# Kernel tuning notes

Hardware: AMD Instinct MI355X
Metric: run time of the kernel (lower is better)

## Reference

```python
import jax, jax.numpy as jnp
import numpy as np

N_E = 16384
E_DIM = 256
BETA = 0.25


def setup_inputs() -> dict:
    key = jax.random.key(0)
    k1, k2 = jax.random.split(key)
    z = jax.random.normal(k1, (8, E_DIM, 32, 32), dtype=jnp.float32)
    embedding = jax.random.uniform(
        k2, (N_E, E_DIM), dtype=jnp.float32, minval=-1.0 / N_E, maxval=1.0 / N_E
    )
    return {"z": z, "embedding": embedding}


def reference(z, embedding):
    # b c h w -> b h w c
    zc = jnp.transpose(z, (0, 2, 3, 1))
    b, h, w, c = zc.shape
    z_flat = zc.reshape(-1, c)  # [N, e_dim]

    # squared-distance matrix: ||z||^2 + ||e||^2 - 2 z e^T  -> [N, n_e]
    d = (
        jnp.sum(z_flat * z_flat, axis=1, keepdims=True)
        + jnp.sum(embedding * embedding, axis=1)
        - 2.0 * jnp.einsum("nd,kd->nk", z_flat, embedding)
    )
    idx = jnp.argmin(d, axis=1)  # [N]

    z_q = embedding[idx].reshape(b, h, w, c)

    sg = jax.lax.stop_gradient
    # legacy=True loss: mse(sg(z_q), z) + beta * mse(z_q, sg(z))
    loss = jnp.mean((sg(z_q) - zc) ** 2) + BETA * jnp.mean((z_q - sg(zc)) ** 2)

    # straight-through estimator
    z_q_st = zc + sg(z_q - zc)
    z_q_out = jnp.transpose(z_q_st, (0, 3, 1, 2))  # b h w c -> b c h w
    return z_q_out, loss, idx
```

## Files before the change

### kernel.cpp

```cpp
#include <hip/hip_runtime.h>

#define E_DIM  256
#define N_E    16384
#define N_ROWS 8192
#define HW     1024
#define NPART  128

typedef _Float16 f16x8 __attribute__((ext_vector_type(8)));
typedef float    f32x4 __attribute__((ext_vector_type(4)));

#define ESCALE   1048576.0f
#define UNSCALE  1.9073486328125e-6f

#define ROR_DPP(v, CTRL) \
  ((unsigned)__builtin_amdgcn_update_dpp(0, (int)(v), (CTRL), 0xF, 0xF, false))

__device__ __forceinline__ float score_ref32(const float* zr,
                                             const float* __restrict__ E,
                                             const float* __restrict__ eNorm,
                                             int idx, float zn) {
  const float4* e4p = (const float4*)(E + (size_t)idx * E_DIM);
  float d0 = 0.f, d1 = 0.f, d2 = 0.f, d3 = 0.f;
#pragma unroll 16
  for (int q = 0; q < 64; ++q) {
    float4 e4 = e4p[q];
    d0 = fmaf(zr[q * 4 + 0], e4.x, d0);
    d1 = fmaf(zr[q * 4 + 1], e4.y, d1);
    d2 = fmaf(zr[q * 4 + 2], e4.z, d2);
    d3 = fmaf(zr[q * 4 + 3], e4.w, d3);
  }
  float dot = (d0 + d1) + (d2 + d3);
  float base = zn + eNorm[idx];
  float td = 2.0f * dot;
  return base - td;
}

#define ZB_Z    256
#define EB_E    512
__global__ __launch_bounds__(256) void k_prep(const float* __restrict__ z,
                                              const float* __restrict__ E,
                                              _Float16* __restrict__ Ah,
                                              _Float16* __restrict__ Bh,
                                              float* __restrict__ eNorm,
                                              float* __restrict__ zNorm,
                                              float* __restrict__ zL1,
                                              float* __restrict__ out_loss) {
#pragma clang fp contract(off)
  const int bi = blockIdx.x, t = threadIdx.x;

  if (bi < ZB_Z) {
    __shared__ float sLZ[256][32];
    __shared__ float sN2[16][32];
    __shared__ float sL1[16][32];
    const int n0 = bi * 32;
    const int b = n0 >> 10, hw0 = n0 & 1023;

    {
      const int nl = t & 31, cs = t >> 5;
      const float* zb = z + (size_t)b * E_DIM * HW + hw0 + nl;
#pragma unroll 4
      for (int it = 0; it < 32; ++it) {
        int c = it * 8 + cs;
        sLZ[c][nl] = zb[(size_t)c * HW];
      }
    }
    __syncthreads();

    {
      const int nl = t & 31, seg = t >> 5;
      const int n = n0 + nl;
      const int perm = (n >> 1) & 3;
#pragma unroll
      for (int u = 0; u < 4; ++u) {
        const int c0 = seg * 32 + u * 8;
        f16x8 hh;
#pragma unroll
        for (int j = 0; j < 8; ++j) hh[j] = (_Float16)sLZ[c0 + j][nl];
        size_t dst = (size_t)seg * (N_ROWS * 32) + (size_t)n * 32 + (size_t)(u ^ perm) * 8;
        *(f16x8*)&Ah[dst] = hh;
      }
    }

#pragma unroll
    for (int it = 0; it < 2; ++it) {
      int task = it * 256 + t;
      int nl = task & 31, c16 = task >> 5;
      int h = c16 >> 3, j = c16 & 7;
      float r2 = 0.f, r1 = 0.f;
#pragma unroll
      for (int i = 0; i < 16; ++i) {
        float v = sLZ[h * 128 + i * 8 + j][nl];
        r2 = r2 + v * v;
        r1 = r1 + fabsf(v);
      }
      sN2[c16][nl] = r2;
      sL1[c16][nl] = r1;
    }
    __syncthreads();
    if (t < 32) {
      float q[16], p[16];
#pragma unroll
      for (int c16 = 0; c16 < 16; ++c16) { q[c16] = sN2[c16][t]; p[c16] = sL1[c16][t]; }
      float h0 = ((q[0] + q[1]) + (q[2] + q[3])) + ((q[4] + q[5]) + (q[6] + q[7]));
      float h1 = ((q[8] + q[9]) + (q[10] + q[11])) + ((q[12] + q[13]) + (q[14] + q[15]));
      zNorm[n0 + t] = h0 + h1;
      float g0 = ((p[0] + p[1]) + (p[2] + p[3])) + ((p[4] + p[5]) + (p[6] + p[7]));
      float g1 = ((p[8] + p[9]) + (p[10] + p[11])) + ((p[12] + p[13]) + (p[14] + p[15]));
      zL1[n0 + t] = g0 + g1;
    }
  } else {
    __shared__ float sNP[8][32];
    const int be = bi - ZB_Z;
    if (be == 0 && t == 0) out_loss[0] = 0.f;
    const int kc = t >> 5, rl = t & 31;
    const int k = be * 32 + rl;
    const int perm = (k >> 1) & 3;
    const float* src = E + (size_t)k * E_DIM + kc * 32;

    float4 v4[8];
#pragma unroll
    for (int u2 = 0; u2 < 8; ++u2) v4[u2] = ((const float4*)src)[u2];

    float nsum = 0.f;
    size_t base = (size_t)kc * (N_E * 32) + (size_t)k * 32;
#pragma unroll
    for (int u = 0; u < 4; ++u) {
      float v[8] = {v4[u * 2].x, v4[u * 2].y, v4[u * 2].z, v4[u * 2].w,
                    v4[u * 2 + 1].x, v4[u * 2 + 1].y, v4[u * 2 + 1].z, v4[u * 2 + 1].w};
      f16x8 hh;
#pragma unroll
      for (int j = 0; j < 8; ++j) {
        nsum = nsum + v[j] * v[j];
        hh[j] = (_Float16)(v[j] * ESCALE);
      }
      *(f16x8*)&Bh[base + (size_t)(u ^ perm) * 8] = hh;
    }
    sNP[kc][rl] = nsum;
    __syncthreads();
    if (t < 32) {
      float s = 0.f;
#pragma unroll
      for (int kc2 = 0; kc2 < 8; ++kc2) s += sNP[kc2][t];
      eNorm[be * 32 + t] = s;
    }
  }
}

__global__ __launch_bounds__(128, 2) void k_scores_mfma(
    const _Float16* __restrict__ Ah, const _Float16* __restrict__ Bh,
    const float* __restrict__ eNorm,
    unsigned* __restrict__ pK1, unsigned* __restrict__ pK2,
    unsigned* __restrict__ pK3) {
#pragma clang fp contract(off)
  const int mt = blockIdx.x, nt = blockIdx.y;
  const int m0 = mt * 128, n0 = nt * 128;

  const int t = threadIdx.x;
  const int lane = t & 63, w = t >> 6;
  const int tx = lane & 15, quad = lane >> 4;
  const int wm = w * 64;
  const int swz = (quad ^ ((tx >> 1) & 3)) * 8;

  const size_t planeA = (size_t)N_ROWS * 32, planeB = (size_t)N_E * 32;
  const size_t baseA = (size_t)(m0 + wm + tx) * 32 + swz;
  const size_t baseB = (size_t)(n0 + tx) * 32 + swz;

  f32x4 acc[4][8];
#pragma unroll
  for (int i = 0; i < 4; ++i)
#pragma unroll
    for (int j = 0; j < 8; ++j) acc[i][j] = (f32x4){0.f, 0.f, 0.f, 0.f};

#pragma unroll
  for (int kc = 0; kc < 8; ++kc) {
    f16x8 ah[4], bh[8];
#pragma unroll
    for (int i = 0; i < 4; ++i)
      ah[i] = *(const f16x8*)&Ah[kc * planeA + baseA + (size_t)i * 512];
#pragma unroll
    for (int j = 0; j < 8; ++j)
      bh[j] = *(const f16x8*)&Bh[kc * planeB + baseB + (size_t)j * 512];

    __builtin_amdgcn_s_setprio(1);
#pragma unroll
    for (int j = 0; j < 8; ++j)
#pragma unroll
      for (int i = 0; i < 4; ++i)
        acc[i][j] = __builtin_amdgcn_mfma_f32_16x16x32_f16(ah[i], bh[j], acc[i][j], 0, 0, 0);
    __builtin_amdgcn_s_setprio(0);
  }

  float enq[8];
#pragma unroll
  for (int j = 0; j < 8; ++j)
    enq[j] = fmaf(eNorm[n0 + j * 16 + tx], 2097152.f, 131072.f);

#pragma unroll
  for (int i = 0; i < 4; ++i) {
#pragma unroll
    for (int r = 0; r < 4; ++r) {
      const int rloc = wm + i * 16 + quad * 4 + r;
      unsigned k[8];
#pragma unroll
      for (int j = 0; j < 8; ++j) {
        float tq = fmaf(acc[i][j][r], -4.0f, enq[j]);
        k[j] = (((unsigned)tq) << 14) | (unsigned)(n0 + j * 16 + tx);
      }
      unsigned a = min(k[0], k[1]), b = max(k[0], k[1]);
      unsigned c = min(k[2], k[3]), d = max(k[2], k[3]);
      unsigned a1 = min(a, c), e0 = max(a, c), f0 = min(b, d);
      unsigned a2 = min(e0, f0), a3 = max(e0, f0);
      a = min(k[4], k[5]); b = max(k[4], k[5]);
      c = min(k[6], k[7]); d = max(k[6], k[7]);
      unsigned b1 = min(a, c); e0 = max(a, c); f0 = min(b, d);
      unsigned b2 = min(e0, f0), b3 = max(e0, f0);
      unsigned m1 = min(a1, b1);
      unsigned m2 = min(max(a1, b1), min(a2, b2));
      unsigned m3 = min(min(a3, b3), min(max(a2, b1), max(a1, b2)));
#define MERGE_R(CTRL)                                              \
      {                                                            \
        unsigned o1 = ROR_DPP(m1, CTRL);                           \
        unsigned o2 = ROR_DPP(m2, CTRL);                           \
        unsigned o3 = ROR_DPP(m3, CTRL);                           \
        unsigned n1 = min(m1, o1);                                 \
        unsigned n2 = min(max(m1, o1), min(m2, o2));               \
        unsigned n3 = min(min(m3, o3), min(max(m2, o1), max(m1, o2))); \
        m1 = n1; m2 = n2; m3 = n3;                                 \
      }
      MERGE_R(0x121)
      MERGE_R(0x122)
      MERGE_R(0x124)
      MERGE_R(0x128)
#undef MERGE_R
      if (tx == 0) {
        const size_t o = (size_t)nt * N_ROWS + m0 + rloc;
        pK1[o] = m1;
        pK2[o] = m2;
        pK3[o] = m3;
      }
    }
  }
}

__global__ __launch_bounds__(1024) void k_post(
    const unsigned* __restrict__ pK1, const unsigned* __restrict__ pK2,
    const unsigned* __restrict__ pK3,
    const float* __restrict__ zL1, const float* __restrict__ zNorm,
    const float* __restrict__ z, const float* __restrict__ E,
    const float* __restrict__ eNorm,
    float* __restrict__ out, float* __restrict__ out_loss,
    float* __restrict__ out_idx) {
#pragma clang fp contract(off)
  __shared__ float zc[32][264];
  __shared__ unsigned sM[32][32];
  __shared__ unsigned gK[32];
  __shared__ int   fI[32];
  __shared__ int   cand[32][16];
  __shared__ int   ccnt[32];
  __shared__ int   heavy[32][4];
  __shared__ int   hcnt[32];
  __shared__ float fS[32][32];
  __shared__ int   fiS[32][32];
  __shared__ float wsum[16];

  const int t = threadIdx.x;
  const int r = t & 31, s = t >> 5;
  const int n0 = blockIdx.x * 32;
  const int n = n0 + r;
  const int b = n >> 10, hw = n & 1023;

  if (t < 32) { ccnt[t] = 0; hcnt[t] = 0; }

  {
    const float* zrow = z + ((size_t)b * E_DIM + s * 8) * HW + hw;
#pragma unroll
    for (int k = 0; k < 8; ++k) zc[r][s * 8 + k] = zrow[(size_t)k * HW];
  }

  unsigned mk = 0xFFFFFFFFu;
#pragma unroll
  for (int i = 0; i < 4; ++i) {
    int ti = s * 4 + i;
    mk = min(mk, pK1[(size_t)ti * N_ROWS + n]);
  }
  sM[s][r] = mk;
  __syncthreads();
  if (t < 32) {
    unsigned bk = sM[0][t];
#pragma unroll
    for (int s3 = 1; s3 < 32; ++s3) bk = min(bk, sM[s3][t]);
    gK[t] = bk;
  }
  __syncthreads();

  {
    const unsigned qW =
        (unsigned)(fmaf(zL1[n], 2.384185791015625e-7f, 8e-5f) * 2097152.f) + 3u;
    unsigned thrq = (gK[r] >> 14) + qW;
    if (thrq > 262143u) thrq = 262143u;
    const unsigned thrk = (thrq << 14) | 0x3FFFu;
#pragma unroll
    for (int i = 0; i < 4; ++i) {
      int ti = s * 4 + i;
      size_t o = (size_t)ti * N_ROWS + n;
      unsigned k1 = pK1[o], k2 = pK2[o], k3 = pK3[o];
      if (k1 <= thrk) { int p = atomicAdd(&ccnt[r], 1); if (p < 16) cand[r][p] = (int)(k1 & 0x3FFFu); }
      if (k2 <= thrk) { int p = atomicAdd(&ccnt[r], 1); if (p < 16) cand[r][p] = (int)(k2 & 0x3FFFu); }
      if (k3 <= thrk) { int p = atomicAdd(&hcnt[r], 1); if (p < 4)  heavy[r][p] = ti; }
    }
  }
  __syncthreads();

  {
    const int rcnt = ccnt[r], rhc = hcnt[r];
    const bool ovf = (rcnt > 16) || (rhc > 4);
    const bool ex = (rcnt > 1) || (rhc > 0);
    float bv = 3.4e38f;
    int bi = 0x7fffffff;
    if (ex) {
      const float zn = zNorm[n];
      if (ovf) {
        for (int k = s; k < N_E; k += 32) {
          float sp = score_ref32(&zc[r][0], E, eNorm, k, zn);
          if (sp < bv || (sp == bv && k < bi)) { bv = sp; bi = k; }
        }
      } else {
        for (int c = s; c < rcnt; c += 32) {
          int idx = cand[r][c];
          float sp = score_ref32(&zc[r][0], E, eNorm, idx, zn);
          if (sp < bv || (sp == bv && idx < bi)) { bv = sp; bi = idx; }
        }
        for (int h = 0; h < rhc; ++h) {
          int ti = heavy[r][h];
          for (int cc = s; cc < 128; cc += 32) {
            int idx = ti * 128 + cc;
            float sp = score_ref32(&zc[r][0], E, eNorm, idx, zn);
            if (sp < bv || (sp == bv && idx < bi)) { bv = sp; bi = idx; }
          }
        }
      }
    }
    fS[r][s] = bv;
    fiS[r][s] = bi;
  }
  __syncthreads();
  if (t < 32) {
    const int rcnt = ccnt[t], rhc = hcnt[t];
    int fidx;
    if (rcnt <= 1 && rhc == 0) {
      fidx = (int)(gK[t] & 0x3FFFu);
    } else {
      float bv = fS[t][0];
      int bi = fiS[t][0];
#pragma unroll
      for (int s3 = 1; s3 < 32; ++s3) {
        float v = fS[t][s3];
        int id = fiS[t][s3];
        if (v < bv || (v == bv && id < bi)) { bv = v; bi = id; }
      }
      fidx = bi;
    }
    fI[t] = fidx;
    out_idx[n0 + t] = (float)fidx;
  }
  __syncthreads();

  const int idx = fI[r];
  const float4* erow4 = (const float4*)(E + (size_t)idx * E_DIM + s * 8);
  float* orow = out + ((size_t)b * E_DIM + s * 8) * HW + hw;
  float acc = 0.f;
#pragma unroll
  for (int c4 = 0; c4 < 2; ++c4) {
    float4 e4 = erow4[c4];
    float ev[4] = {e4.x, e4.y, e4.z, e4.w};
#pragma unroll
    for (int j2 = 0; j2 < 4; ++j2) {
      int c = c4 * 4 + j2;
      float zv = zc[r][s * 8 + c];
      orow[(size_t)c * HW] = ev[j2];
      float d = ev[j2] - zv;
      acc = fmaf(d, d, acc);
    }
  }
  for (int off = 32; off > 0; off >>= 1) acc += __shfl_down(acc, off, 64);
  if ((t & 63) == 0) wsum[t >> 6] = acc;
  __syncthreads();
  if (t == 0) {
    float s0 = 0.f;
#pragma unroll
    for (int wv = 0; wv < 16; ++wv) s0 += wsum[wv];
    atomicAdd(out_loss, s0 * (1.25f / 2097152.f));
  }
}

extern "C" void kernel_launch(void* const* d_in, const int* in_sizes, int n_in,
                              void* d_out, int out_size, void* d_ws, size_t ws_size,
                              hipStream_t stream) {
  const float* z = (const float*)d_in[0];
  const float* E = (const float*)d_in[1];
  float* out = (float*)d_out;
  float* out_loss = out + 2097152;
  float* out_idx = out + 2097153;

  _Float16* Ah = (_Float16*)d_ws;
  _Float16* Bh = Ah + (size_t)N_ROWS * E_DIM;
  float* eNorm = (float*)(Bh + (size_t)N_E * E_DIM);
  float* zL1 = eNorm + N_E;
  float* zNorm = zL1 + N_ROWS;
  unsigned* pK1 = (unsigned*)(zNorm + N_ROWS);
  unsigned* pK2 = pK1 + (size_t)NPART * N_ROWS;
  unsigned* pK3 = pK2 + (size_t)NPART * N_ROWS;

  k_prep<<<ZB_Z + EB_E, 256, 0, stream>>>(z, E, Ah, Bh, eNorm, zNorm, zL1, out_loss);
  k_scores_mfma<<<dim3(N_ROWS / 128, N_E / 128), 128, 0, stream>>>(
      Ah, Bh, eNorm, pK1, pK2, pK3);
  k_post<<<N_ROWS / 32, 1024, 0, stream>>>(
      pK1, pK2, pK3, zL1, zNorm, z, E, eNorm, out, out_loss, out_idx);
}
```

Baseline: 176.8 us.

## Transpose MFMA operands so top-3 reduction runs in-lane before cross-quad shuffles

Swaps the A and B operands of the MFMA so each lane's accumulator registers hold four consecutive codebook columns for one z row, rather than four rows for one column. The top-3 selection then runs mostly inside each lane across j and the four accumulator elements. Only two xor shuffles across quads are needed per 16-row block, replacing four DPP row-rotate merges for each of 16 row slots. The embedding norms are now read as float4 per j, and the partial-result stores are issued once per i instead of once per (i,r). The cost is that ds_swizzle/bpermute-style shuffles replace cheaper DPP moves.

```diff
diff --git a/kernel.cpp b/kernel.cpp
--- a/kernel.cpp
+++ b/kernel.cpp
@@ -12,8 +12,13 @@
 #define ESCALE   1048576.0f
 #define UNSCALE  1.9073486328125e-6f
 
-#define ROR_DPP(v, CTRL) \
-  ((unsigned)__builtin_amdgcn_update_dpp(0, (int)(v), (CTRL), 0xF, 0xF, false))
+#define MERGE3(m1, m2, m3, t1, t2, t3)                       \
+  {                                                          \
+    unsigned n1 = min(m1, t1);                               \
+    unsigned n2 = min(max(m1, t1), min(m2, t2));             \
+    unsigned n3 = min(min(m3, t3), min(max(m2, t1), max(m1, t2))); \
+    m1 = n1; m2 = n2; m3 = n3;                               \
+  }
 
 __device__ __forceinline__ float score_ref32(const float* zr,
                                              const float* __restrict__ E,
@@ -186,58 +191,49 @@
     for (int j = 0; j < 8; ++j)
 #pragma unroll
       for (int i = 0; i < 4; ++i)
-        acc[i][j] = __builtin_amdgcn_mfma_f32_16x16x32_f16(ah[i], bh[j], acc[i][j], 0, 0, 0);
+        acc[i][j] = __builtin_amdgcn_mfma_f32_16x16x32_f16(bh[j], ah[i], acc[i][j], 0, 0, 0);
     __builtin_amdgcn_s_setprio(0);
   }
 
-  float enq[8];
-#pragma unroll
-  for (int j = 0; j < 8; ++j)
-    enq[j] = fmaf(eNorm[n0 + j * 16 + tx], 2097152.f, 131072.f);
-
+  const unsigned colb = (unsigned)(n0 + quad * 4);
 #pragma unroll
   for (int i = 0; i < 4; ++i) {
-#pragma unroll
-    for (int r = 0; r < 4; ++r) {
-      const int rloc = wm + i * 16 + quad * 4 + r;
-      unsigned k[8];
-#pragma unroll
-      for (int j = 0; j < 8; ++j) {
-        float tq = fmaf(acc[i][j][r], -4.0f, enq[j]);
-        k[j] = (((unsigned)tq) << 14) | (unsigned)(n0 + j * 16 + tx);
-      }
-      unsigned a = min(k[0], k[1]), b = max(k[0], k[1]);
-      unsigned c = min(k[2], k[3]), d = max(k[2], k[3]);
-      unsigned a1 = min(a, c), e0 = max(a, c), f0 = min(b, d);
-      unsigned a2 = min(e0, f0), a3 = max(e0, f0);
-      a = min(k[4], k[5]); b = max(k[4], k[5]);
-      c = min(k[6], k[7]); d = max(k[6], k[7]);
-      unsigned b1 = min(a, c); e0 = max(a, c); f0 = min(b, d);
-      unsigned b2 = min(e0, f0), b3 = max(e0, f0);
-      unsigned m1 = min(a1, b1);
-      unsigned m2 = min(max(a1, b1), min(a2, b2));
-      unsigned m3 = min(min(a3, b3), min(max(a2, b1), max(a1, b2)));
-#define MERGE_R(CTRL)                                              \
-      {                                                            \
-        unsigned o1 = ROR_DPP(m1, CTRL);                           \
-        unsigned o2 = ROR_DPP(m2, CTRL);                           \
-        unsigned o3 = ROR_DPP(m3, CTRL);                           \
-        unsigned n1 = min(m1, o1);                                 \
-        unsigned n2 = min(max(m1, o1), min(m2, o2));               \
-        unsigned n3 = min(min(m3, o3), min(max(m2, o1), max(m1, o2))); \
-        m1 = n1; m2 = n2; m3 = n3;                                 \
-      }
-      MERGE_R(0x121)
-      MERGE_R(0x122)
-      MERGE_R(0x124)
-      MERGE_R(0x128)
-#undef MERGE_R
-      if (tx == 0) {
-        const size_t o = (size_t)nt * N_ROWS + m0 + rloc;
-        pK1[o] = m1;
-        pK2[o] = m2;
-        pK3[o] = m3;
-      }
+    unsigned m1 = 0xFFFFFFFFu, m2 = 0xFFFFFFFFu, m3 = 0xFFFFFFFFu;
+#pragma unroll
+    for (int j = 0; j < 8; ++j) {
+      float4 e4 = ((const float4*)(eNorm + n0 + j * 16))[quad];
+      unsigned kk[4];
+      {
+        float q0 = fmaf(e4.x, 2097152.f, 131072.f);
+        float q1 = fmaf(e4.y, 2097152.f, 131072.f);
+        float q2 = fmaf(e4.z, 2097152.f, 131072.f);
+        float q3 = fmaf(e4.w, 2097152.f, 131072.f);
+        kk[0] = (((unsigned)fmaf(acc[i][j][0], -4.0f, q0)) << 14) | (colb + j * 16 + 0);
+        kk[1] = (((unsigned)fmaf(acc[i][j][1], -4.0f, q1)) << 14) | (colb + j * 16 + 1);
+        kk[2] = (((unsigned)fmaf(acc[i][j][2], -4.0f, q2)) << 14) | (colb + j * 16 + 2);
+        kk[3] = (((unsigned)fmaf(acc[i][j][3], -4.0f, q3)) << 14) | (colb + j * 16 + 3);
+      }
+      unsigned a = min(kk[0], kk[1]), b = max(kk[0], kk[1]);
+      unsigned c = min(kk[2], kk[3]), d = max(kk[2], kk[3]);
+      unsigned t1 = min(a, c), e0 = max(a, c), f0 = min(b, d);
+      unsigned t2 = min(e0, f0), t3 = max(e0, f0);
+      MERGE3(m1, m2, m3, t1, t2, t3)
+    }
+    {
+      unsigned o1 = (unsigned)__shfl_xor((int)m1, 16, 64);
+      unsigned o2 = (unsigned)__shfl_xor((int)m2, 16, 64);
+      unsigned o3 = (unsigned)__shfl_xor((int)m3, 16, 64);
+      MERGE3(m1, m2, m3, o1, o2, o3)
+      o1 = (unsigned)__shfl_xor((int)m1, 32, 64);
+      o2 = (unsigned)__shfl_xor((int)m2, 32, 64);
+      o3 = (unsigned)__shfl_xor((int)m3, 32, 64);
+      MERGE3(m1, m2, m3, o1, o2, o3)
+    }
+    if (quad == 0) {
+      const size_t o = (size_t)nt * N_ROWS + m0 + wm + i * 16 + tx;
+      pK1[o] = m1;
+      pK2[o] = m2;
+      pK3[o] = m3;
     }
   }
 }
```

New measurement: 174.8 us. About the same (-1.1%).
